# Kernel tuning notes

Measured on AMD Instinct MI355X. Metric: run time of the kernel, lower is better.

Reference implementation:

```python
import jax, jax.numpy as jnp
import numpy as np

D = 512          # embedding_dim (cfg.hidden_size)
K = 1024         # codebook_size
DECAY = 0.99
EPS = 1e-05
COMMITMENT_COST = 0.25


def setup_inputs() -> dict:
    key = jax.random.key(0)
    k1, k2, k3 = jax.random.split(key, 3)
    return {
        "inputs": jax.random.normal(k1, (32, 1024, D), dtype=jnp.float32),
        "embedding_weight": jax.random.normal(k2, (K, D), dtype=jnp.float32),
        "ema_cluster_size": jnp.zeros((K,), dtype=jnp.float32),
        "ema_w": jax.random.normal(k3, (K, D), dtype=jnp.float32),
    }


def reference(inputs, embedding_weight, ema_cluster_size, ema_w):
    input_shape = inputs.shape
    flat = inputs.reshape(-1, D)  # [N, D]

    # Squared L2 distances to every codebook entry: [N, K]
    distances = (
        jnp.sum(flat ** 2, axis=1, keepdims=True)
        + jnp.sum(embedding_weight ** 2, axis=1)
        - 2.0 * flat @ embedding_weight.T
    )
    idx = jnp.argmin(distances, axis=1)                      # [N]
    encodings = jax.nn.one_hot(idx, K, dtype=flat.dtype)     # [N, K]

    # ---- EMA codebook update (training path) ----
    counts = jnp.sum(encodings, axis=0)                      # == bincount(idx)
    new_cs = ema_cluster_size * DECAY + (1.0 - DECAY) * counts
    n = jnp.sum(new_cs)
    new_cs = (new_cs + EPS) / (n + K * EPS) * n              # Laplace smoothing
    # dw = encodings.T @ flat, done as a fused gather-reduce instead of dense matmul
    dw = jax.ops.segment_sum(flat, idx, num_segments=K)      # [K, D]
    new_ema_w = ema_w * DECAY + (1.0 - DECAY) * dw
    new_embedding = new_ema_w / new_cs[:, None]              # updated codebook

    # quantized = encodings @ new_embedding, expressed as a gather
    quantized = new_embedding[idx].reshape(input_shape)

    e_latent_loss = jnp.mean((jax.lax.stop_gradient(quantized) - inputs) ** 2)
    loss = COMMITMENT_COST * e_latent_loss

    # straight-through estimator
    quantized = inputs + jax.lax.stop_gradient(quantized - inputs)

    avg_probs = jnp.mean(encodings, axis=0)
    perplexity = jnp.exp(-jnp.sum(avg_probs * jnp.log(avg_probs + 1e-10)))
    return (loss, quantized, perplexity, encodings)
```

## Files before the change

kernel.cpp:

```cpp
#include <hip/hip_runtime.h>

#define NROWS 32768
#define DIM   512
#define KC    1024

typedef __attribute__((ext_vector_type(8)))  short short8v;
typedef __attribute__((ext_vector_type(16))) float f32x16;

#define AS1 __attribute__((address_space(1)))
#define AS3 __attribute__((address_space(3)))

__device__ __forceinline__ void split_bf16(float v, short& hi, short& lo) {
    unsigned u = __float_as_uint(v);
    unsigned r = u + 0x7FFFu + ((u >> 16) & 1u);
    hi = (short)(r >> 16);
    float hif = __uint_as_float(r & 0xFFFF0000u);
    float rem = v - hif;
    unsigned u2 = __float_as_uint(rem);
    unsigned r2 = u2 + 0x7FFFu + ((u2 >> 16) & 1u);
    lo = (short)(r2 >> 16);
}

__device__ __forceinline__ void conv8(const float4 a, const float4 b,
                                      short8v& hi, short8v& lo) {
    short h, l;
    split_bf16(a.x, h, l); hi[0] = h; lo[0] = l;
    split_bf16(a.y, h, l); hi[1] = h; lo[1] = l;
    split_bf16(a.z, h, l); hi[2] = h; lo[2] = l;
    split_bf16(a.w, h, l); hi[3] = h; lo[3] = l;
    split_bf16(b.x, h, l); hi[4] = h; lo[4] = l;
    split_bf16(b.y, h, l); hi[5] = h; lo[5] = l;
    split_bf16(b.z, h, l); hi[6] = h; lo[6] = l;
    split_bf16(b.w, h, l); hi[7] = h; lo[7] = l;
}

__device__ __forceinline__ unsigned long long pack_key(float d, int c) {
    unsigned u = __float_as_uint(d);
    u = (u & 0x80000000u) ? ~u : (u | 0x80000000u);
    return ((unsigned long long)u << 32) | (unsigned)c;
}

__global__ __launch_bounds__(256) void k_eprep(const float* __restrict__ E,
                                               short* __restrict__ efrag,
                                               float* __restrict__ en2,
                                               int* __restrict__ counts,
                                               unsigned long long* __restrict__ packed) {
    __shared__ short hbuf[32][520];
    __shared__ short lbuf[32][520];
    int b = blockIdx.x, t = threadIdx.x;
    const float* src = E + (size_t)b * 32 * DIM;
    short* dst = efrag + (size_t)b * 32768;

    unsigned long long* p = packed + b * 1024;
    #pragma unroll
    for (int i = 0; i < 4; ++i) p[t + i * 256] = 0xFFFFFFFFFFFFFFFFull;
    if (b == 0) {
        #pragma unroll
        for (int i = 0; i < 4; ++i) counts[t + i * 256] = 0;
    }

    #pragma unroll
    for (int f = 0; f < 16; ++f) {
        int u = t + f * 256;
        int row = u >> 7, c4 = (u & 127) * 4;
        float4 v = *reinterpret_cast<const float4*>(&src[row * DIM + c4]);
        short4 h4, l4;
        split_bf16(v.x, h4.x, l4.x); split_bf16(v.y, h4.y, l4.y);
        split_bf16(v.z, h4.z, l4.z); split_bf16(v.w, h4.w, l4.w);
        *reinterpret_cast<short4*>(&hbuf[row][c4]) = h4;
        *reinterpret_cast<short4*>(&lbuf[row][c4]) = l4;
    }
    __syncthreads();
    #pragma unroll
    for (int f = 0; f < 16; ++f) {
        int u = t + f * 256;
        int lane = u & 63, h = (u >> 6) & 1, kb = u >> 7;
        int row = lane & 31, k0 = kb * 16 + (lane >> 5) * 8;
        const short* s = h ? &lbuf[row][k0] : &hbuf[row][k0];
        short8v val = *reinterpret_cast<const short8v*>(s);
        *reinterpret_cast<short8v*>(&dst[(size_t)u * 8]) = val;
    }

    int w = t >> 6, lane = t & 63;
    for (int cc = 0; cc < 8; ++cc) {
        int c = b * 32 + w * 8 + cc;
        const float* row = E + (size_t)c * DIM;
        float4 a = *reinterpret_cast<const float4*>(&row[lane * 8]);
        float4 bb = *reinterpret_cast<const float4*>(&row[lane * 8 + 4]);
        float s = a.x*a.x + a.y*a.y + a.z*a.z + a.w*a.w
                + bb.x*bb.x + bb.y*bb.y + bb.z*bb.z + bb.w*bb.w;
        #pragma unroll
        for (int off = 32; off; off >>= 1) s += __shfl_xor(s, off);
        if (!lane) en2[c] = s;
    }
}

__global__ __launch_bounds__(256, 2) void k_argmin(const float* __restrict__ x,
                                                   const short* __restrict__ efrag,
                                                   const float* __restrict__ en2,
                                                   unsigned long long* __restrict__ packed) {
    __shared__ short sbuf[4][2][8][512];
    const int tid = threadIdx.x;
    const int w = tid >> 6, l = tid & 63;
    const int wr = w >> 1, wc = w & 1;
    const int l31 = l & 31, lh = l >> 5;

    int bid = blockIdx.x;
    int xcd = bid & 7, j = bid >> 3;
    int row0 = (xcd * 32 + (j >> 2)) * 128;
    int c0   = (j & 3) * 256;

    const float* axsrc[2];
    #pragma unroll
    for (int m = 0; m < 2; ++m)
        axsrc[m] = x + (size_t)(row0 + wr * 64 + m * 32 + l31) * DIM + lh * 8;
    const short* gsrc[4];
    #pragma unroll
    for (int n = 0; n < 4; ++n)
        gsrc[n] = efrag + (size_t)(c0 / 32 + wc * 4 + n) * 32768 + l * 8;

    f32x16 acc[2][4];
    #pragma unroll
    for (int a = 0; a < 2; ++a)
        #pragma unroll
        for (int b = 0; b < 4; ++b)
            #pragma unroll
            for (int r = 0; r < 16; ++r) acc[a][b][r] = 0.f;

    short8v ah0[2], al0[2], ah1[2], al1[2];

    {
        float4 p0[2], p1[2];
        #pragma unroll
        for (int m = 0; m < 2; ++m) {
            p0[m] = *reinterpret_cast<const float4*>(axsrc[m]);
            p1[m] = *reinterpret_cast<const float4*>(axsrc[m] + 4);
        }
        #pragma unroll
        for (int n = 0; n < 4; ++n) {
            __builtin_amdgcn_global_load_lds((const AS1 void*)gsrc[n],
                                             (AS3 void*)&sbuf[w][0][n * 2 + 0][0], 16, 0, 0);
            __builtin_amdgcn_global_load_lds((const AS1 void*)(gsrc[n] + 512),
                                             (AS3 void*)&sbuf[w][0][n * 2 + 1][0], 16, 0, 0);
        }
        conv8(p0[0], p1[0], ah0[0], al0[0]);
        conv8(p0[1], p1[1], ah0[1], al0[1]);
    }

#define KITER(KB, AHC, ALC, AHN, ALN, CUR, NXT, PREF)                          \
    {                                                                          \
        asm volatile("s_waitcnt vmcnt(0)" ::: "memory");                       \
        float4 r0[2], r1[2];                                                   \
        if (PREF) {                                                            \
            _Pragma("unroll")                                                  \
            for (int m = 0; m < 2; ++m) {                                      \
                r0[m] = *reinterpret_cast<const float4*>(axsrc[m] + ((KB) + 1) * 16);     \
                r1[m] = *reinterpret_cast<const float4*>(axsrc[m] + ((KB) + 1) * 16 + 4); \
            }                                                                  \
            _Pragma("unroll")                                                  \
            for (int n = 0; n < 4; ++n) {                                      \
                __builtin_amdgcn_global_load_lds(                              \
                    (const AS1 void*)(gsrc[n] + (size_t)((KB) + 1) * 1024),    \
                    (AS3 void*)&sbuf[w][NXT][n * 2 + 0][0], 16, 0, 0);         \
                __builtin_amdgcn_global_load_lds(                              \
                    (const AS1 void*)(gsrc[n] + (size_t)((KB) + 1) * 1024 + 512), \
                    (AS3 void*)&sbuf[w][NXT][n * 2 + 1][0], 16, 0, 0);         \
            }                                                                  \
        }                                                                      \
        short8v bh[4], bl[4];                                                  \
        _Pragma("unroll")                                                      \
        for (int n = 0; n < 4; ++n) {                                          \
            bh[n] = *reinterpret_cast<const short8v*>(&sbuf[w][CUR][n * 2 + 0][l * 8]); \
            bl[n] = *reinterpret_cast<const short8v*>(&sbuf[w][CUR][n * 2 + 1][l * 8]); \
        }                                                                      \
        _Pragma("unroll")                                                      \
        for (int m = 0; m < 2; ++m) {                                          \
            _Pragma("unroll")                                                  \
            for (int n = 0; n < 4; ++n) {                                      \
                acc[m][n] = __builtin_amdgcn_mfma_f32_32x32x16_bf16(AHC[m], bh[n], acc[m][n], 0, 0, 0); \
                acc[m][n] = __builtin_amdgcn_mfma_f32_32x32x16_bf16(AHC[m], bl[n], acc[m][n], 0, 0, 0); \
                acc[m][n] = __builtin_amdgcn_mfma_f32_32x32x16_bf16(ALC[m], bh[n], acc[m][n], 0, 0, 0); \
            }                                                                  \
        }                                                                      \
        if (PREF) {                                                            \
            conv8(r0[0], r1[0], AHN[0], ALN[0]);                               \
            conv8(r0[1], r1[1], AHN[1], ALN[1]);                               \
        }                                                                      \
    }

    for (int kp = 0; kp < 14; ++kp) {
        const int kbe = kp * 2, kbo = kp * 2 + 1;
        KITER(kbe, ah0, al0, ah1, al1, 0, 1, 1);
        KITER(kbo, ah1, al1, ah0, al0, 1, 0, 1);
    }
    KITER(28, ah0, al0, ah1, al1, 0, 1, 1);
    KITER(29, ah1, al1, ah0, al0, 1, 0, 1);
    KITER(30, ah0, al0, ah1, al1, 0, 1, 1);
    KITER(31, ah1, al1, ah0, al0, 1, 0, 0);
#undef KITER

    float e2[4];
    #pragma unroll
    for (int n = 0; n < 4; ++n) e2[n] = en2[c0 + wc * 128 + n * 32 + l31];
    #pragma unroll
    for (int m = 0; m < 2; ++m) {
        #pragma unroll
        for (int r = 0; r < 16; ++r) {
            unsigned long long key = 0xFFFFFFFFFFFFFFFFull;
            #pragma unroll
            for (int n = 0; n < 4; ++n) {
                float d = fmaf(-2.f, acc[m][n][r], e2[n]);
                unsigned long long k = pack_key(d, c0 + wc * 128 + n * 32 + l31);
                if (k < key) key = k;
            }
            #pragma unroll
            for (int off = 1; off < 32; off <<= 1) {
                unsigned long long o = __shfl_xor(key, off);
                if (o < key) key = o;
            }
            if (l31 == 0) {
                int grow = row0 + wr * 64 + m * 32 + (r & 3) + 8 * (r >> 2) + 4 * lh;
                atomicMin(&packed[grow], key);
            }
        }
    }
}

__global__ __launch_bounds__(256) void k_hist(const unsigned long long* __restrict__ packed,
                                              int* __restrict__ idx,
                                              int* __restrict__ counts) {
    __shared__ int h[KC];
    for (int i = threadIdx.x; i < KC; i += 256) h[i] = 0;
    __syncthreads();
    int g = blockIdx.x * 256 + threadIdx.x;
    int c = (int)(unsigned)(packed[g] & 0xFFFFFFFFull);
    idx[g] = c;
    atomicAdd(&h[c], 1);
    __syncthreads();
    for (int i = threadIdx.x; i < KC; i += 256)
        if (h[i]) atomicAdd(&counts[i], h[i]);
}

__global__ __launch_bounds__(1024) void k_meta(const int* __restrict__ counts,
                                               const float* __restrict__ ema_cs,
                                               float* __restrict__ smoothed,
                                               int* __restrict__ offsets,
                                               int* __restrict__ cursor,
                                               float* __restrict__ perp_out) {
    __shared__ float ws1[16], ws2[16];
    __shared__ int wsum[16];
    int t = threadIdx.x, lane = t & 63, w = t >> 6;
    int cnt = counts[t];
    float cs = ema_cs[t] * 0.99f + 0.01f * (float)cnt;
    float p = (float)cnt / 32768.f;
    float v1 = cs, v2 = p * logf(p + 1e-10f);
    #pragma unroll
    for (int off = 32; off; off >>= 1) {
        v1 += __shfl_xor(v1, off);
        v2 += __shfl_xor(v2, off);
    }
    int s = cnt;
    #pragma unroll
    for (int off = 1; off < 64; off <<= 1) {
        int u = __shfl_up(s, off);
        if (lane >= off) s += u;
    }
    if (lane == 0) { ws1[w] = v1; ws2[w] = v2; }
    if (lane == 63) wsum[w] = s;
    __syncthreads();
    float n = 0.f;
    #pragma unroll
    for (int i = 0; i < 16; ++i) n += ws1[i];
    smoothed[t] = (cs + 1e-5f) / (n + 1024.f * 1e-5f) * n;
    if (t == 0) {
        float sp = 0.f;
        #pragma unroll
        for (int i = 0; i < 16; ++i) sp += ws2[i];
        perp_out[0] = expf(-sp);
    }
    int wo = 0;
    for (int i = 0; i < 16; ++i) if (i < w) wo += wsum[i];
    int off_ = wo + s - cnt;
    offsets[t] = off_;
    cursor[t] = off_;
}

__global__ __launch_bounds__(256) void k_scatter(const int* __restrict__ idx,
                                                 int* __restrict__ cursor,
                                                 int* __restrict__ bucket) {
    int g = blockIdx.x * 256 + threadIdx.x;
    int c = idx[g];
    int pos = atomicAdd(&cursor[c], 1);
    bucket[pos] = g;
}

__global__ __launch_bounds__(256) void k_dw(const float* __restrict__ x,
                                            const float* __restrict__ ema_w,
                                            const int* __restrict__ offsets,
                                            const int* __restrict__ counts,
                                            const int* __restrict__ bucket,
                                            const float* __restrict__ smoothed,
                                            float* __restrict__ newE) {
    __shared__ int rows[256];
    int k = blockIdx.x >> 1, half = blockIdx.x & 1, t = threadIdx.x;
    int d = half * 256 + t;
    int beg = offsets[k], m = counts[k];
    float a = 0.f;
    for (int base = 0; base < m; base += 256) {
        int n = min(256, m - base);
        __syncthreads();
        if (t < n) rows[t] = bucket[beg + base + t];
        __syncthreads();
        int i = 0;
        for (; i + 4 <= n; i += 4) {
            float v0 = x[(size_t)rows[i]     * DIM + d];
            float v1 = x[(size_t)rows[i + 1] * DIM + d];
            float v2 = x[(size_t)rows[i + 2] * DIM + d];
            float v3 = x[(size_t)rows[i + 3] * DIM + d];
            a += v0 + v1 + v2 + v3;
        }
        for (; i < n; ++i) a += x[(size_t)rows[i] * DIM + d];
    }
    newE[(size_t)k * DIM + d] =
        (ema_w[(size_t)k * DIM + d] * 0.99f + 0.01f * a) / smoothed[k];
}

__global__ __launch_bounds__(256) void k_qe(const float* __restrict__ x,
                                            const int* __restrict__ idx,
                                            const float* __restrict__ newE,
                                            float* __restrict__ outq,
                                            float* __restrict__ enc,
                                            float* __restrict__ partials) {
    int b = blockIdx.x, t = threadIdx.x;
    int row8 = b * 8;
    float lp = 0.f;
    #pragma unroll
    for (int it = 0; it < 4; ++it) {
        int slot = t + it * 256;
        int r = slot >> 7;
        int c4 = (slot & 127) * 4;
        int row = row8 + r;
        int code = idx[row];
        float4 in = *reinterpret_cast<const float4*>(&x[(size_t)row * DIM + c4]);
        float4 q  = *reinterpret_cast<const float4*>(&newE[(size_t)code * DIM + c4]);
        float4 d;
        d.x = q.x - in.x; d.y = q.y - in.y; d.z = q.z - in.z; d.w = q.w - in.w;
        float4 o;
        o.x = in.x + d.x; o.y = in.y + d.y; o.z = in.z + d.z; o.w = in.w + d.w;
        *reinterpret_cast<float4*>(&outq[(size_t)row * DIM + c4]) = o;
        lp += d.x*d.x + d.y*d.y + d.z*d.z + d.w*d.w;
    }
    {
        int er = row8 + (t >> 5);
        int l32 = t & 31;
        int one = idx[er];
        float4* dst = reinterpret_cast<float4*>(enc + (size_t)er * KC);
        #pragma unroll
        for (int s = 0; s < 8; ++s) {
            int c4 = l32 + s * 32;
            int base = c4 * 4;
            float4 v;
            v.x = (one == base)     ? 1.f : 0.f;
            v.y = (one == base + 1) ? 1.f : 0.f;
            v.z = (one == base + 2) ? 1.f : 0.f;
            v.w = (one == base + 3) ? 1.f : 0.f;
            dst[c4] = v;
        }
    }
    #pragma unroll
    for (int off = 32; off; off >>= 1) lp += __shfl_xor(lp, off);
    __shared__ float wr[4];
    int lane = t & 63, w = t >> 6;
    if (!lane) wr[w] = lp;
    __syncthreads();
    if (t == 0) partials[b] = wr[0] + wr[1] + wr[2] + wr[3];
}

__global__ __launch_bounds__(256) void k_lossfin(const float* __restrict__ partials,
                                                 float* __restrict__ out0) {
    __shared__ double red[256];
    double s = 0.0;
    for (int i = threadIdx.x; i < 4096; i += 256) s += (double)partials[i];
    red[threadIdx.x] = s; __syncthreads();
    for (int st = 128; st; st >>= 1) {
        if (threadIdx.x < st) red[threadIdx.x] += red[threadIdx.x + st];
        __syncthreads();
    }
    if (!threadIdx.x) out0[0] = (float)(0.25 * red[0] / 16777216.0);
}

extern "C" void kernel_launch(void* const* d_in, const int* in_sizes, int n_in,
                              void* d_out, int out_size, void* d_ws, size_t ws_size,
                              hipStream_t stream) {
    const float* x   = (const float*)d_in[0];
    const float* E   = (const float*)d_in[1];
    const float* ecs = (const float*)d_in[2];
    const float* emw = (const float*)d_in[3];
    float* out = (float*)d_out;

    char* ws = (char*)d_ws;
    int*   idx      = (int*)(ws + 0);
    int*   bucket   = (int*)(ws + 131072);
    float* en2      = (float*)(ws + 262144);
    int*   counts   = (int*)(ws + 266240);
    int*   offsets  = (int*)(ws + 270336);
    int*   cursor   = (int*)(ws + 274432);
    float* smoothed = (float*)(ws + 278528);
    float* newE     = (float*)(ws + 282624);
    float* partials = (float*)(ws + 282624 + 2097152);
    unsigned long long* packed = (unsigned long long*)newE;

    float* out_loss = out;
    float* out_q    = out + 1;
    float* out_perp = out + 16777217;
    float* out_enc  = out + 16777218;

    short* efrag = (short*)out_enc;

    k_eprep  <<<KC / 32, 256, 0, stream>>>(E, efrag, en2, counts, packed);
    k_argmin <<<(NROWS / 128) * 4, 256, 0, stream>>>(x, efrag, en2, packed);
    k_hist   <<<NROWS / 256, 256, 0, stream>>>(packed, idx, counts);
    k_meta   <<<1, 1024, 0, stream>>>(counts, ecs, smoothed, offsets, cursor, out_perp);
    k_scatter<<<NROWS / 256, 256, 0, stream>>>(idx, cursor, bucket);
    k_dw     <<<KC * 2, 256, 0, stream>>>(x, emw, offsets, counts, bucket, smoothed, newE);
    k_qe     <<<NROWS / 8, 256, 0, stream>>>(x, idx, newE, out_q, out_enc, partials);
    k_lossfin<<<1, 256, 0, stream>>>(partials, out_loss);
}
```

Baseline: 312.5 us.

## Restructure argmin GEMM into 256x256 block tiles with shared LDS operands

The argmin kernel moves from 4-wave blocks, where each wave privately staged its own codebook fragments, to 8-wave blocks covering 256 rows by 256 codes. The converted bf16 hi/lo input rows and the codebook fragments now live in shared LDS buffers (double-buffered A, triple-buffered B) that all waves read, so each global load is reused across waves rather than duplicated. This adds a block-wide barrier every k-step and raises s_setprio around the MFMA section. The goal is less global and L2 traffic per MFMA, at the cost of synchronisation and more LDS per block.

```diff
diff --git a/kernel.cpp b/kernel.cpp
--- a/kernel.cpp
+++ b/kernel.cpp
@@ -95,122 +95,122 @@
     }
 }
 
-__global__ __launch_bounds__(256, 2) void k_argmin(const float* __restrict__ x,
+__global__ __launch_bounds__(512, 2) void k_argmin(const float* __restrict__ x,
                                                    const short* __restrict__ efrag,
                                                    const float* __restrict__ en2,
                                                    unsigned long long* __restrict__ packed) {
-    __shared__ short sbuf[4][2][8][512];
+    __shared__ short sA[2][8][2][512];
+    __shared__ short sB[3][8][2][512];
     const int tid = threadIdx.x;
     const int w = tid >> 6, l = tid & 63;
-    const int wr = w >> 1, wc = w & 1;
+    const int wr = w >> 2, wc = w & 3;
     const int l31 = l & 31, lh = l >> 5;
 
     int bid = blockIdx.x;
     int xcd = bid & 7, j = bid >> 3;
-    int row0 = (xcd * 32 + (j >> 2)) * 128;
+    int row0 = (xcd * 16 + (j >> 2)) * 256;
     int c0   = (j & 3) * 256;
 
-    const float* axsrc[2];
-    #pragma unroll
-    for (int m = 0; m < 2; ++m)
-        axsrc[m] = x + (size_t)(row0 + wr * 64 + m * 32 + l31) * DIM + lh * 8;
-    const short* gsrc[4];
-    #pragma unroll
-    for (int n = 0; n < 4; ++n)
-        gsrc[n] = efrag + (size_t)(c0 / 32 + wc * 4 + n) * 32768 + l * 8;
-
-    f32x16 acc[2][4];
-    #pragma unroll
-    for (int a = 0; a < 2; ++a)
-        #pragma unroll
-        for (int b = 0; b < 4; ++b)
+    const float* axsrc = x + (size_t)(row0 + w * 32 + l31) * DIM + lh * 8;
+    const short* gsrc = efrag + (size_t)(c0 / 32 + w) * 32768 + l * 8;
+
+    f32x16 acc[4][2];
+    #pragma unroll
+    for (int a = 0; a < 4; ++a)
+        #pragma unroll
+        for (int b = 0; b < 2; ++b)
             #pragma unroll
             for (int r = 0; r < 16; ++r) acc[a][b][r] = 0.f;
 
-    short8v ah0[2], al0[2], ah1[2], al1[2];
-
+    float4 ra0, ra1;
+    ra0 = *reinterpret_cast<const float4*>(axsrc);
+    ra1 = *reinterpret_cast<const float4*>(axsrc + 4);
+    __builtin_amdgcn_sched_barrier(0);
+    __builtin_amdgcn_global_load_lds((const AS1 void*)gsrc,
+                                     (AS3 void*)&sB[0][w][0][0], 16, 0, 0);
+    __builtin_amdgcn_global_load_lds((const AS1 void*)(gsrc + 512),
+                                     (AS3 void*)&sB[0][w][1][0], 16, 0, 0);
+    __builtin_amdgcn_sched_barrier(0);
+    asm volatile("s_waitcnt vmcnt(2)" ::: "memory");
     {
-        float4 p0[2], p1[2];
-        #pragma unroll
-        for (int m = 0; m < 2; ++m) {
-            p0[m] = *reinterpret_cast<const float4*>(axsrc[m]);
-            p1[m] = *reinterpret_cast<const float4*>(axsrc[m] + 4);
-        }
-        #pragma unroll
-        for (int n = 0; n < 4; ++n) {
-            __builtin_amdgcn_global_load_lds((const AS1 void*)gsrc[n],
-                                             (AS3 void*)&sbuf[w][0][n * 2 + 0][0], 16, 0, 0);
-            __builtin_amdgcn_global_load_lds((const AS1 void*)(gsrc[n] + 512),
-                                             (AS3 void*)&sbuf[w][0][n * 2 + 1][0], 16, 0, 0);
-        }
-        conv8(p0[0], p1[0], ah0[0], al0[0]);
-        conv8(p0[1], p1[1], ah0[1], al0[1]);
-    }
-
-#define KITER(KB, AHC, ALC, AHN, ALN, CUR, NXT, PREF)                          \
-    {                                                                          \
-        asm volatile("s_waitcnt vmcnt(0)" ::: "memory");                       \
-        float4 r0[2], r1[2];                                                   \
-        if (PREF) {                                                            \
-            _Pragma("unroll")                                                  \
-            for (int m = 0; m < 2; ++m) {                                      \
-                r0[m] = *reinterpret_cast<const float4*>(axsrc[m] + ((KB) + 1) * 16);     \
-                r1[m] = *reinterpret_cast<const float4*>(axsrc[m] + ((KB) + 1) * 16 + 4); \
-            }                                                                  \
-            _Pragma("unroll")                                                  \
-            for (int n = 0; n < 4; ++n) {                                      \
-                __builtin_amdgcn_global_load_lds(                              \
-                    (const AS1 void*)(gsrc[n] + (size_t)((KB) + 1) * 1024),    \
-                    (AS3 void*)&sbuf[w][NXT][n * 2 + 0][0], 16, 0, 0);         \
-                __builtin_amdgcn_global_load_lds(                              \
-                    (const AS1 void*)(gsrc[n] + (size_t)((KB) + 1) * 1024 + 512), \
-                    (AS3 void*)&sbuf[w][NXT][n * 2 + 1][0], 16, 0, 0);         \
-            }                                                                  \
-        }                                                                      \
-        short8v bh[4], bl[4];                                                  \
-        _Pragma("unroll")                                                      \
-        for (int n = 0; n < 4; ++n) {                                          \
-            bh[n] = *reinterpret_cast<const short8v*>(&sbuf[w][CUR][n * 2 + 0][l * 8]); \
-            bl[n] = *reinterpret_cast<const short8v*>(&sbuf[w][CUR][n * 2 + 1][l * 8]); \
-        }                                                                      \
-        _Pragma("unroll")                                                      \
-        for (int m = 0; m < 2; ++m) {                                          \
-            _Pragma("unroll")                                                  \
-            for (int n = 0; n < 4; ++n) {                                      \
-                acc[m][n] = __builtin_amdgcn_mfma_f32_32x32x16_bf16(AHC[m], bh[n], acc[m][n], 0, 0, 0); \
-                acc[m][n] = __builtin_amdgcn_mfma_f32_32x32x16_bf16(AHC[m], bl[n], acc[m][n], 0, 0, 0); \
-                acc[m][n] = __builtin_amdgcn_mfma_f32_32x32x16_bf16(ALC[m], bh[n], acc[m][n], 0, 0, 0); \
-            }                                                                  \
-        }                                                                      \
-        if (PREF) {                                                            \
-            conv8(r0[0], r1[0], AHN[0], ALN[0]);                               \
-            conv8(r0[1], r1[1], AHN[1], ALN[1]);                               \
-        }                                                                      \
-    }
-
-    for (int kp = 0; kp < 14; ++kp) {
-        const int kbe = kp * 2, kbo = kp * 2 + 1;
-        KITER(kbe, ah0, al0, ah1, al1, 0, 1, 1);
-        KITER(kbo, ah1, al1, ah0, al0, 1, 0, 1);
-    }
-    KITER(28, ah0, al0, ah1, al1, 0, 1, 1);
-    KITER(29, ah1, al1, ah0, al0, 1, 0, 1);
-    KITER(30, ah0, al0, ah1, al1, 0, 1, 1);
-    KITER(31, ah1, al1, ah0, al0, 1, 0, 0);
-#undef KITER
-
-    float e2[4];
-    #pragma unroll
-    for (int n = 0; n < 4; ++n) e2[n] = en2[c0 + wc * 128 + n * 32 + l31];
-    #pragma unroll
-    for (int m = 0; m < 2; ++m) {
+        short8v hi, lo; conv8(ra0, ra1, hi, lo);
+        *reinterpret_cast<short8v*>(&sA[0][w][0][l * 8]) = hi;
+        *reinterpret_cast<short8v*>(&sA[0][w][1][l * 8]) = lo;
+    }
+
+    for (int kb = 0; kb < 32; ++kb) {
+        const int curA = kb & 1, curB = kb % 3;
+        float4 rn0, rn1;
+        if (kb < 31) {
+            const int nxtA = curA ^ 1, nxtB = (kb + 1) % 3;
+            rn0 = *reinterpret_cast<const float4*>(axsrc + (kb + 1) * 16);
+            rn1 = *reinterpret_cast<const float4*>(axsrc + (kb + 1) * 16 + 4);
+            __builtin_amdgcn_sched_barrier(0);
+            __builtin_amdgcn_global_load_lds(
+                (const AS1 void*)(gsrc + (size_t)(kb + 1) * 1024),
+                (AS3 void*)&sB[nxtB][w][0][0], 16, 0, 0);
+            __builtin_amdgcn_global_load_lds(
+                (const AS1 void*)(gsrc + (size_t)(kb + 1) * 1024 + 512),
+                (AS3 void*)&sB[nxtB][w][1][0], 16, 0, 0);
+            __builtin_amdgcn_sched_barrier(0);
+            asm volatile("s_waitcnt vmcnt(4) lgkmcnt(0)" ::: "memory");
+        } else {
+            asm volatile("s_waitcnt vmcnt(0) lgkmcnt(0)" ::: "memory");
+        }
+        __builtin_amdgcn_s_barrier();
+        __builtin_amdgcn_sched_barrier(0);
+
+        {
+            short8v ah[4], al[4], bh[2], bl[2];
+            const short* pa = &sA[curA][0][0][0];
+            const short* pb = &sB[curB][0][0][0];
+            #pragma unroll
+            for (int m = 0; m < 4; ++m) {
+                int g = wr * 4 + m;
+                ah[m] = *reinterpret_cast<const short8v*>(pa + (g * 2 + 0) * 512 + l * 8);
+                al[m] = *reinterpret_cast<const short8v*>(pa + (g * 2 + 1) * 512 + l * 8);
+            }
+            #pragma unroll
+            for (int n = 0; n < 2; ++n) {
+                int g = wc * 2 + n;
+                bh[n] = *reinterpret_cast<const short8v*>(pb + (g * 2 + 0) * 512 + l * 8);
+                bl[n] = *reinterpret_cast<const short8v*>(pb + (g * 2 + 1) * 512 + l * 8);
+            }
+            __builtin_amdgcn_s_setprio(1);
+            #pragma unroll
+            for (int m = 0; m < 4; ++m)
+                #pragma unroll
+                for (int n = 0; n < 2; ++n) {
+                    acc[m][n] = __builtin_amdgcn_mfma_f32_32x32x16_bf16(
+                        ah[m], bh[n], acc[m][n], 0, 0, 0);
+                    acc[m][n] = __builtin_amdgcn_mfma_f32_32x32x16_bf16(
+                        ah[m], bl[n], acc[m][n], 0, 0, 0);
+                    acc[m][n] = __builtin_amdgcn_mfma_f32_32x32x16_bf16(
+                        al[m], bh[n], acc[m][n], 0, 0, 0);
+                }
+            __builtin_amdgcn_s_setprio(0);
+        }
+
+        if (kb < 31) {
+            asm volatile("s_waitcnt vmcnt(2)" ::: "memory");
+            short8v hi, lo; conv8(rn0, rn1, hi, lo);
+            *reinterpret_cast<short8v*>(&sA[curA ^ 1][w][0][l * 8]) = hi;
+            *reinterpret_cast<short8v*>(&sA[curA ^ 1][w][1][l * 8]) = lo;
+        }
+    }
+
+    float e2[2];
+    #pragma unroll
+    for (int n = 0; n < 2; ++n) e2[n] = en2[c0 + wc * 64 + n * 32 + l31];
+    #pragma unroll
+    for (int m = 0; m < 4; ++m) {
         #pragma unroll
         for (int r = 0; r < 16; ++r) {
             unsigned long long key = 0xFFFFFFFFFFFFFFFFull;
             #pragma unroll
-            for (int n = 0; n < 4; ++n) {
+            for (int n = 0; n < 2; ++n) {
                 float d = fmaf(-2.f, acc[m][n][r], e2[n]);
-                unsigned long long k = pack_key(d, c0 + wc * 128 + n * 32 + l31);
+                unsigned long long k = pack_key(d, c0 + wc * 64 + n * 32 + l31);
                 if (k < key) key = k;
             }
             #pragma unroll
@@ -219,7 +219,7 @@
                 if (o < key) key = o;
             }
             if (l31 == 0) {
-                int grow = row0 + wr * 64 + m * 32 + (r & 3) + 8 * (r >> 2) + 4 * lh;
+                int grow = row0 + wr * 128 + m * 32 + (r & 3) + 8 * (r >> 2) + 4 * lh;
                 atomicMin(&packed[grow], key);
             }
         }
@@ -418,7 +418,7 @@
     short* efrag = (short*)out_enc;
 
     k_eprep  <<<KC / 32, 256, 0, stream>>>(E, efrag, en2, counts, packed);
-    k_argmin <<<(NROWS / 128) * 4, 256, 0, stream>>>(x, efrag, en2, packed);
+    k_argmin <<<(NROWS / 256) * 4, 512, 0, stream>>>(x, efrag, en2, packed);
     k_hist   <<<NROWS / 256, 256, 0, stream>>>(packed, idx, counts);
     k_meta   <<<1, 1024, 0, stream>>>(counts, ecs, smoothed, offsets, cursor, out_perp);
     k_scatter<<<NROWS / 256, 256, 0, stream>>>(idx, cursor, bucket);
```

After: 315.9 us. About the same (+1.1%).
